# Performance work log

Hardware: AMD Instinct MI355X
Metric: run time of the kernel (lower is better)

The kernel has to match this reference:

```python
import jax, jax.numpy as jnp
import numpy as np

N = 50000      # nodes
E = 800000     # edges
IN_C = 128
HID = 96
OUT_C = 40
L = 8          # num_layers
ALPHA = 0.1
THETA = 0.5
DROPOUT = 0.5


def setup_inputs() -> dict:
    key = jax.random.key(0)
    ks = jax.random.split(key, 6)
    x = jax.random.normal(ks[0], (N, IN_C), dtype=jnp.float32)
    edge_index = jax.random.randint(ks[1], (2, E), 0, N, dtype=jnp.int64)
    proj_w = jax.random.normal(ks[2], (IN_C, HID), dtype=jnp.float32) / np.sqrt(IN_C)
    proj_b = jnp.zeros((HID,), dtype=jnp.float32)
    conv_ws = jax.random.normal(ks[3], (L, HID, HID), dtype=jnp.float32) / np.sqrt(HID)
    out_w = jax.random.normal(ks[4], (2 * HID, OUT_C), dtype=jnp.float32) / np.sqrt(2 * HID)
    out_b = jnp.zeros((OUT_C,), dtype=jnp.float32)
    return {"x": x, "edge_index": edge_index, "proj_w": proj_w, "proj_b": proj_b,
            "conv_ws": conv_ws, "out_w": out_w, "out_b": out_b}


def reference(x, edge_index, proj_w, proj_b, conv_ws, out_w, out_b):
    # --- GCN normalization with self loops (computed once, as GCN2Conv caches it) ---
    loops = jnp.arange(N, dtype=edge_index.dtype)
    src = jnp.concatenate([edge_index[0], loops])   # [E+N]
    dst = jnp.concatenate([edge_index[1], loops])
    deg = jax.ops.segment_sum(jnp.ones(E + N, dtype=x.dtype), dst, num_segments=N)
    dis = jax.lax.rsqrt(deg)                        # deg >= 1 due to self loops
    norm = dis[src] * dis[dst]                      # [E+N]

    h0 = x @ proj_w + proj_b                        # [N, HID]
    h = h0
    key = jax.random.key(42)
    for k in range(L):
        delta = 1.0 / 2 ** k
        kq, ke, kd, key = jax.random.split(key, 4)
        # dithered quantization
        b = (jax.random.uniform(kq, h.shape, dtype=h.dtype) - 0.5) * delta
        h_q = jnp.floor((h + b) / delta) * delta - b
        # GCN2Conv: propagate + initial residual + identity mapping (shared weights)
        agg = jax.ops.segment_sum(h_q[src] * norm[:, None], dst, num_segments=N)
        t = (1.0 - ALPHA) * agg + ALPHA * h0
        beta = float(np.log(THETA / (k + 1) + 1.0))
        h = (1.0 - beta) * t + beta * (t @ conv_ws[k])
        # gaussian noise + relu
        h = jax.nn.relu(h + 0.01 * jax.random.normal(ke, h.shape, dtype=h.dtype))
        if k != L - 1:
            keep = 1.0 - DROPOUT
            mask = jax.random.bernoulli(kd, keep, h.shape)
            h = jnp.where(mask, h / keep, 0.0)
    return jnp.concatenate([h0, h], axis=-1) @ out_w + out_b
```

## Files before the change

### kernel.cpp

```cpp
#include <hip/hip_runtime.h>
#include <hip/hip_fp16.h>
#include <cstdint>
#include <cmath>

#define HID 96
#define INC 128
#define OUTC 40

__device__ __forceinline__ unsigned rotl32d(unsigned x, int r){ return (x<<r)|(x>>(32-r)); }

__device__ __forceinline__ void tf2x32_dev(unsigned k0, unsigned k1, unsigned x0, unsigned x1,
                                           unsigned &y0, unsigned &y1){
  unsigned ks2 = k0 ^ k1 ^ 0x1BD11BDAu;
  x0 += k0; x1 += k1;
#define TFR(r) { x0 += x1; x1 = rotl32d(x1, r); x1 ^= x0; }
  TFR(13) TFR(15) TFR(26) TFR(6)   x0 += k1;  x1 += ks2 + 1u;
  TFR(17) TFR(29) TFR(16) TFR(24)  x0 += ks2; x1 += k0 + 2u;
  TFR(13) TFR(15) TFR(26) TFR(6)   x0 += k0;  x1 += k1 + 3u;
  TFR(17) TFR(29) TFR(16) TFR(24)  x0 += k1;  x1 += ks2 + 4u;
  TFR(13) TFR(15) TFR(26) TFR(6)   x0 += ks2; x1 += k0 + 5u;
#undef TFR
  y0 = x0; y1 = x1;
}

__device__ __forceinline__ unsigned tf_bits(unsigned k0, unsigned k1, unsigned idx){
  unsigned y0, y1; tf2x32_dev(k0, k1, 0u, idx, y0, y1); return y0 ^ y1;
}

__device__ __forceinline__ float u01_from_bits(unsigned bits){
  return __uint_as_float((bits >> 9) | 0x3f800000u) - 1.0f;
}

__device__ __forceinline__ float erfinv_xla(float x){
  float w = -log1pf(-x*x);
  float p;
  if (w < 5.0f){
    w = w - 2.5f;
    p = 2.81022636e-08f;
    p = fmaf(p,w, 3.43273939e-07f);
    p = fmaf(p,w,-3.5233877e-06f);
    p = fmaf(p,w,-4.39150654e-06f);
    p = fmaf(p,w, 0.00021858087f);
    p = fmaf(p,w,-0.00125372503f);
    p = fmaf(p,w,-0.00417768164f);
    p = fmaf(p,w, 0.246640727f);
    p = fmaf(p,w, 1.50140941f);
  } else {
    w = sqrtf(w) - 3.0f;
    p = -0.000200214257f;
    p = fmaf(p,w, 0.000100950558f);
    p = fmaf(p,w, 0.00134934322f);
    p = fmaf(p,w,-0.00367342844f);
    p = fmaf(p,w, 0.00573950773f);
    p = fmaf(p,w,-0.0076224613f);
    p = fmaf(p,w, 0.00943887047f);
    p = fmaf(p,w, 1.00167406f);
    p = fmaf(p,w, 2.83297682f);
  }
  return p*x;
}

__global__ void k_detect(const unsigned* __restrict__ raw, int* flag){
  unsigned v = raw[2*threadIdx.x + 1];
  unsigned long long m = __ballot(v == 0u);
  if (threadIdx.x == 0) *flag = (m == 0xFFFFFFFFFFFFFFFFull) ? 1 : 0;
}

__global__ void k_convcount(const unsigned* __restrict__ raw, const int* __restrict__ flag,
                            int E, int* __restrict__ src, int* __restrict__ dst,
                            int* __restrict__ cnt){
  int e = blockIdx.x*256 + threadIdx.x; if (e >= E) return;
  int s, d;
  if (*flag){ s = (int)raw[2*(size_t)e]; d = (int)raw[2*((size_t)E + e)]; }
  else      { const int* r = (const int*)raw; s = r[e]; d = r[E + e]; }
  src[e] = s; dst[e] = d;
  atomicAdd(&cnt[d], 1);
}

__global__ void k_psum_histo(const int* __restrict__ cnt, int N,
                             int* __restrict__ psum, int* __restrict__ bcnt){
  __shared__ int sh[256];
  __shared__ int lh[64];
  int tid = threadIdx.x; int n = blockIdx.x*256 + tid;
  int v = (n < N) ? cnt[n] : 0;
  sh[tid] = v;
  if (tid < 64) lh[tid] = 0;
  __syncthreads();
  if (n < N) atomicAdd(&lh[min(v, 63)], 1);
  for (int off = 128; off > 0; off >>= 1){
    __syncthreads();
    if (tid < off) sh[tid] += sh[tid + off];
  }
  __syncthreads();
  if (tid == 0) psum[blockIdx.x] = sh[0];
  if (tid < 64){
    int c = lh[tid];
    if (c > 0) atomicAdd(&bcnt[tid], c);
  }
}

__global__ void k_scan2(int* __restrict__ psum, int nb, int* __restrict__ bcnt){
  __shared__ int sh[256];
  __shared__ int sb[64];
  int tid = threadIdx.x;
  int v = (tid < nb) ? psum[tid] : 0;
  sh[tid] = v;
  if (tid < 64) sb[tid] = bcnt[tid];
  __syncthreads();
  for (int off = 1; off < 256; off <<= 1){
    int t = (tid >= off) ? sh[tid - off] : 0;
    __syncthreads();
    sh[tid] += t;
    __syncthreads();
  }
  if (tid < nb) psum[tid] = sh[tid] - v;
  if (tid < 64){
    int off = 0;
    for (int b2 = tid+1; b2 < 64; b2++) off += sb[b2];
    bcnt[tid] = off;
  }
}

__global__ void k_rowptr_perm(const int* __restrict__ cnt, const int* __restrict__ psum,
                              int N, int E, int* __restrict__ rowptr, float* __restrict__ dis,
                              int* __restrict__ bcnt, int* __restrict__ perm){
  __shared__ int sh[256];
  __shared__ int lh[64];
  int tid = threadIdx.x; int n = blockIdx.x*256 + tid;
  int v = (n < N) ? cnt[n] : 0;
  sh[tid] = v;
  if (tid < 64) lh[tid] = 0;
  __syncthreads();
  int b = min(v, 63), r = 0;
  if (n < N) r = atomicAdd(&lh[b], 1);
  for (int off = 1; off < 256; off <<= 1){
    int t = (tid >= off) ? sh[tid - off] : 0;
    __syncthreads();
    sh[tid] += t;
    __syncthreads();
  }
  if (n < N){
    rowptr[n] = psum[blockIdx.x] + sh[tid] - v;
    dis[n] = 1.0f / sqrtf((float)(v + 1));
  }
  if (n == N-1) rowptr[N] = E;
  if (tid < 64){
    int c = lh[tid];
    lh[tid] = (c > 0) ? atomicAdd(&bcnt[tid], c) : 0;
  }
  __syncthreads();
  if (n < N) perm[lh[b] + r] = n;
}

__global__ void k_fill(const int* __restrict__ src, const int* __restrict__ dst, int E,
                       const int* __restrict__ rowptr, int* __restrict__ cnt,
                       const float* __restrict__ dis,
                       int* __restrict__ csr_src, float* __restrict__ csr_w){
  int e = blockIdx.x*256 + threadIdx.x; if (e >= E) return;
  int d = dst[e], s = src[e];
  int pos = atomicAdd(&cnt[d], 1);
  int slot = rowptr[d] + pos;
  csr_src[slot] = s;
  csr_w[slot] = dis[s]*dis[d];
}

__global__ __launch_bounds__(256) void k_h0(
  const float* __restrict__ x, const float* __restrict__ W, const float* __restrict__ bias,
  float* __restrict__ h0, __half* __restrict__ hq, unsigned kq0, unsigned kq1, int N)
{
  __shared__ float xs[64*65];
  __shared__ float wsh[64*96];
  int tid = threadIdx.x; int n0 = blockIdx.x*64;
  int cg = tid & 15, ng = tid >> 4; int c0 = cg*6;
  float acc[4][6];
#pragma unroll
  for (int i=0;i<4;i++) for (int j=0;j<6;j++) acc[i][j]=0.f;
  for (int kc=0; kc<2; kc++){
    if (kc) __syncthreads();
    for (int q=tid; q<1536; q+=256)
      ((float4*)wsh)[q] = ((const float4*)(W + kc*64*96))[q];
    for (int q=tid; q<1024; q+=256){
      int g=q*4; int r=g>>6, col=g&63;
      int n=n0+r; int ns = n<N ? n : N-1;
      float4 v = ((const float4*)(x + (size_t)ns*128 + kc*64))[col>>2];
      xs[r*65+col]=v.x; xs[r*65+col+1]=v.y; xs[r*65+col+2]=v.z; xs[r*65+col+3]=v.w;
    }
    __syncthreads();
    for (int k=0;k<64;k++){
      float wv[6];
#pragma unroll
      for (int j=0;j<6;j++) wv[j]=wsh[k*96 + c0 + j];
#pragma unroll
      for (int i=0;i<4;i++){
        float xv = xs[(ng*4+i)*65 + k];
#pragma unroll
        for (int j=0;j<6;j++) acc[i][j] = fmaf(xv, wv[j], acc[i][j]);
      }
    }
  }
#pragma unroll
  for (int i=0;i<4;i++){
    int n = n0 + ng*4 + i; if (n >= N) continue;
#pragma unroll
    for (int j=0;j<6;j++){
      int c = c0 + j; int p = n*96 + c;
      float v = acc[i][j] + bias[c];
      h0[p] = v;
      unsigned bq = tf_bits(kq0, kq1, (unsigned)p);
      float b = u01_from_bits(bq) - 0.5f;
      hq[(size_t)n*96 + c] = __float2half_rn(floorf(v + b) - b);
    }
  }
}

__global__ __launch_bounds__(256, 4) void k_layer(
  const __half* __restrict__ hq_in, const float* __restrict__ h0, const float* __restrict__ dis,
  const int* __restrict__ rowptr, const int* __restrict__ csr_src, const float* __restrict__ csr_w,
  const int* __restrict__ perm, const float* __restrict__ W,
  float betaf, float ombf,
  unsigned ke0, unsigned ke1, unsigned kd0, unsigned kd1,
  unsigned kq0, unsigned kq1, float delta_n, float invdelta_n,
  int do_dropout, int write_h,
  __half* __restrict__ hq_out, float* __restrict__ h_out, int N)
{
  __shared__ float ts[64*100];
  __shared__ float wsh[24*96];
  __shared__ int rowmap[64];
  int tid = threadIdx.x;
  int tx = tid & 31, ty = tid >> 5;
  int n0 = blockIdx.x*64;

  const uint2* hq2 = (const uint2*)hq_in;
  const float4* h04 = (const float4*)h0;

#pragma unroll 1
  for (int pass = 0; pass < 8; pass++){
    int r = pass*8 + ty;
    int row = n0 + r;
    int n = (row < N) ? perm[row] : -1;
    if (tx == 0) rowmap[r] = n;
    if (tx < 24){
      float4 o = make_float4(0.f, 0.f, 0.f, 0.f);
      if (n >= 0){
        float d = dis[n];
        int lo = rowptr[n], hi = rowptr[n+1];
        uint2 sraw = hq2[(size_t)n*24 + tx];
        float2 s01 = __half22float2(*(__half2*)&sraw.x);
        float2 s23 = __half22float2(*(__half2*)&sraw.y);
        float dd = d*d;
        float ax = s01.x*dd, ay = s01.y*dd, az = s23.x*dd, aw = s23.y*dd;
        for (int s = lo; s < hi; s += 8){
          int   sn[8];
          float w[8];
#pragma unroll
          for (int j = 0; j < 8; j++){
            bool hv = (s + j) < hi;
            sn[j] = hv ? csr_src[s + j] : csr_src[s];
            w[j]  = hv ? csr_w[s + j]   : 0.0f;
          }
          uint2 g[8];
#pragma unroll
          for (int j = 0; j < 8; j++) g[j] = hq2[(size_t)sn[j]*24 + tx];
#pragma unroll
          for (int j = 0; j < 8; j++){
            float2 f01 = __half22float2(*(__half2*)&g[j].x);
            float2 f23 = __half22float2(*(__half2*)&g[j].y);
            ax = fmaf(f01.x, w[j], ax); ay = fmaf(f01.y, w[j], ay);
            az = fmaf(f23.x, w[j], az); aw = fmaf(f23.y, w[j], aw);
          }
        }
        float4 hz = h04[(size_t)n*24 + tx];
        o.x = 0.9f*ax + 0.1f*hz.x;
        o.y = 0.9f*ay + 0.1f*hz.y;
        o.z = 0.9f*az + 0.1f*hz.z;
        o.w = 0.9f*aw + 0.1f*hz.w;
      }
      *((float4*)&ts[r*100 + tx*4]) = o;
    }
  }

  int cg = tid & 7, ng = tid >> 3;
  int c0 = cg * 12;
  int r0 = ng * 2;
  float acc[2][12];
#pragma unroll
  for (int i = 0; i < 2; i++)
#pragma unroll
    for (int j = 0; j < 12; j++) acc[i][j] = 0.f;

  for (int chunk = 0; chunk < 4; chunk++){
    __syncthreads();
    for (int q = tid; q < 576; q += 256)
      ((float4*)wsh)[q] = ((const float4*)(W + chunk*24*96))[q];
    __syncthreads();
#pragma unroll 4
    for (int kk = 0; kk < 24; kk++){
      int k = chunk*24 + kk;
      float4 w0 = *((const float4*)&wsh[kk*96 + c0]);
      float4 w1 = *((const float4*)&wsh[kk*96 + c0 + 4]);
      float4 w2 = *((const float4*)&wsh[kk*96 + c0 + 8]);
      float xv0 = ts[r0*100 + k];
      float xv1 = ts[(r0+1)*100 + k];
      acc[0][0] = fmaf(xv0, w0.x, acc[0][0]);  acc[0][1] = fmaf(xv0, w0.y, acc[0][1]);
      acc[0][2] = fmaf(xv0, w0.z, acc[0][2]);  acc[0][3] = fmaf(xv0, w0.w, acc[0][3]);
      acc[0][4] = fmaf(xv0, w1.x, acc[0][4]);  acc[0][5] = fmaf(xv0, w1.y, acc[0][5]);
      acc[0][6] = fmaf(xv0, w1.z, acc[0][6]);  acc[0][7] = fmaf(xv0, w1.w, acc[0][7]);
      acc[0][8] = fmaf(xv0, w2.x, acc[0][8]);  acc[0][9] = fmaf(xv0, w2.y, acc[0][9]);
      acc[0][10]= fmaf(xv0, w2.z, acc[0][10]); acc[0][11]= fmaf(xv0, w2.w, acc[0][11]);
      acc[1][0] = fmaf(xv1, w0.x, acc[1][0]);  acc[1][1] = fmaf(xv1, w0.y, acc[1][1]);
      acc[1][2] = fmaf(xv1, w0.z, acc[1][2]);  acc[1][3] = fmaf(xv1, w0.w, acc[1][3]);
      acc[1][4] = fmaf(xv1, w1.x, acc[1][4]);  acc[1][5] = fmaf(xv1, w1.y, acc[1][5]);
      acc[1][6] = fmaf(xv1, w1.z, acc[1][6]);  acc[1][7] = fmaf(xv1, w1.w, acc[1][7]);
      acc[1][8] = fmaf(xv1, w2.x, acc[1][8]);  acc[1][9] = fmaf(xv1, w2.y, acc[1][9]);
      acc[1][10]= fmaf(xv1, w2.z, acc[1][10]); acc[1][11]= fmaf(xv1, w2.w, acc[1][11]);
    }
  }

  const float LO = __uint_as_float(0xBF7FFFFFu);
#pragma unroll
  for (int i = 0; i < 2; i++){
    int n = rowmap[r0 + i]; if (n < 0) continue;
    float res[12];
#pragma unroll
    for (int j = 0; j < 12; j++){
      int c = c0 + j; int p = n*96 + c;
      float tv = ts[(r0+i)*100 + c];
      float hv = ombf*tv + betaf*acc[i][j];
      unsigned be = tf_bits(ke0, ke1, (unsigned)p);
      float uv = fmaxf(LO, u01_from_bits(be)*2.0f + LO);
      hv += 0.01f * (1.41421356f * erfinv_xla(uv));
      hv = fmaxf(hv, 0.0f);
      if (do_dropout){
        unsigned bd = tf_bits(kd0, kd1, (unsigned)p);
        hv = (bd < 0x80000000u) ? hv*2.0f : 0.0f;
      }
      if (!write_h){
        unsigned bq = tf_bits(kq0, kq1, (unsigned)p);
        float b = (u01_from_bits(bq) - 0.5f)*delta_n;
        hv = floorf((hv + b)*invdelta_n)*delta_n - b;
      }
      res[j] = hv;
    }
    if (write_h){
      float* dst = h_out + (size_t)n*96 + c0;
#pragma unroll
      for (int j4 = 0; j4 < 3; j4++)
        *((float4*)&dst[j4*4]) = make_float4(res[j4*4], res[j4*4+1], res[j4*4+2], res[j4*4+3]);
    } else {
      uint2* dst = (uint2*)(hq_out + (size_t)n*96 + c0);
#pragma unroll
      for (int j4 = 0; j4 < 3; j4++){
        unsigned lo2 = (unsigned)__half_as_ushort(__float2half_rn(res[j4*4+0]))
                     | ((unsigned)__half_as_ushort(__float2half_rn(res[j4*4+1])) << 16);
        unsigned hi2 = (unsigned)__half_as_ushort(__float2half_rn(res[j4*4+2]))
                     | ((unsigned)__half_as_ushort(__float2half_rn(res[j4*4+3])) << 16);
        dst[j4] = make_uint2(lo2, hi2);
      }
    }
  }
}

__global__ __launch_bounds__(256) void k_final(
  const float* __restrict__ h0, const float* __restrict__ h,
  const float* __restrict__ W, const float* __restrict__ bias,
  float* __restrict__ out, int N)
{
  __shared__ float xs[64*97];
  __shared__ float wsh[96*40];
  int tid = threadIdx.x; int n0 = blockIdx.x*64;
  int cg = tid & 7, ng = tid >> 3; int c0 = cg*5;
  float acc[2][5];
#pragma unroll
  for (int i=0;i<2;i++) for (int j=0;j<5;j++) acc[i][j]=0.f;
  for (int ph=0; ph<2; ph++){
    if (ph) __syncthreads();
    const float* xsrc = ph ? h : h0;
    for (int q=tid; q<960; q+=256)
      ((float4*)wsh)[q] = ((const float4*)(W + ph*96*40))[q];
    for (int q=tid; q<1536; q+=256){
      int g=q*4; int r=g/96, col=g%96;
      int n=n0+r; int ns = n<N ? n : N-1;
      float4 v = ((const float4*)(xsrc + (size_t)ns*96))[col>>2];
      xs[r*97+col]=v.x; xs[r*97+col+1]=v.y; xs[r*97+col+2]=v.z; xs[r*97+col+3]=v.w;
    }
    __syncthreads();
    for (int k=0;k<96;k++){
      float wv[5];
#pragma unroll
      for (int j=0;j<5;j++) wv[j]=wsh[k*40 + c0 + j];
#pragma unroll
      for (int i=0;i<2;i++){
        float xv = xs[(ng*2+i)*97 + k];
#pragma unroll
        for (int j=0;j<5;j++) acc[i][j] = fmaf(xv, wv[j], acc[i][j]);
      }
    }
  }
#pragma unroll
  for (int i=0;i<2;i++){
    int n = n0 + ng*2 + i; if (n >= N) continue;
#pragma unroll
    for (int j=0;j<5;j++)
      out[(size_t)n*40 + c0 + j] = acc[i][j] + bias[c0 + j];
  }
}

static void tf_host(uint32_t k0, uint32_t k1, uint32_t x0, uint32_t x1,
                    uint32_t &y0, uint32_t &y1){
  uint32_t ks2 = k0 ^ k1 ^ 0x1BD11BDAu;
  x0 += k0; x1 += k1;
  auto R = [&](int r){ x0 += x1; x1 = (x1<<r)|(x1>>(32-r)); x1 ^= x0; };
  R(13);R(15);R(26);R(6);   x0 += k1;  x1 += ks2 + 1u;
  R(17);R(29);R(16);R(24);  x0 += ks2; x1 += k0 + 2u;
  R(13);R(15);R(26);R(6);   x0 += k0;  x1 += k1 + 3u;
  R(17);R(29);R(16);R(24);  x0 += k1;  x1 += ks2 + 4u;
  R(13);R(15);R(26);R(6);   x0 += ks2; x1 += k0 + 5u;
  y0 = x0; y1 = x1;
}

extern "C" void kernel_launch(void* const* d_in, const int* in_sizes, int n_in,
                              void* d_out, int out_size, void* d_ws, size_t ws_size,
                              hipStream_t stream)
{
  const float*    x       = (const float*)d_in[0];
  const unsigned* eraw    = (const unsigned*)d_in[1];
  const float*    proj_w  = (const float*)d_in[2];
  const float*    proj_b  = (const float*)d_in[3];
  const float*    conv_w  = (const float*)d_in[4];
  const float*    out_w   = (const float*)d_in[5];
  const float*    out_b   = (const float*)d_in[6];
  float* out = (float*)d_out;

  const int N = in_sizes[0] / INC;
  const int E = in_sizes[1] / 2;
  const size_t NH = (size_t)N * HID;

  float*  ws     = (float*)d_ws;
  float*  h0     = ws;
  __half* hqA    = (__half*)(h0 + NH);
  __half* hqB    = hqA + NH;
  float*  hb     = (float*)(hqB + NH);
  float*  dis    = hb + NH;
  int*    cnt    = (int*)(dis + N);
  int*    rowptr = cnt + N;
  int*    csr_src= rowptr + (N + 1);
  float*  csr_w  = (float*)(csr_src + E);
  int*    srcb   = (int*)(csr_w + E);
  int*    dstb   = srcb + E;
  int*    flag   = dstb + E;
  int*    perm   = flag + 1;
  int*    bcnt   = perm + N;
  int*    psum   = bcnt + 64;
  (void)ws_size; (void)n_in; (void)out_size;

  uint32_t kq[8][2], ke[8][2], kd[8][2];
  {
    uint32_t K0 = 0u, K1 = 42u;
    for (int k = 0; k < 8; k++){
      uint32_t y0, y1;
      tf_host(K0, K1, 0u, 0u, y0, y1); kq[k][0]=y0; kq[k][1]=y1;
      tf_host(K0, K1, 0u, 1u, y0, y1); ke[k][0]=y0; ke[k][1]=y1;
      tf_host(K0, K1, 0u, 2u, y0, y1); kd[k][0]=y0; kd[k][1]=y1;
      tf_host(K0, K1, 0u, 3u, y0, y1); K0=y0; K1=y1;
    }
  }

  const int gE  = (E + 255)/256;
  const int gN  = (N + 255)/256;
  const int gMM = (N + 63)/64;

  hipMemsetAsync(cnt, 0, (size_t)N*4, stream);
  hipMemsetAsync(bcnt, 0, 64*4, stream);
  k_detect <<<1, 64, 0, stream>>>(eraw, flag);
  k_convcount<<<gE, 256, 0, stream>>>(eraw, flag, E, srcb, dstb, cnt);
  k_psum_histo<<<gN, 256, 0, stream>>>(cnt, N, psum, bcnt);
  k_scan2  <<<1, 256, 0, stream>>>(psum, gN, bcnt);
  k_rowptr_perm<<<gN, 256, 0, stream>>>(cnt, psum, N, E, rowptr, dis, bcnt, perm);
  hipMemsetAsync(cnt, 0, (size_t)N*4, stream);
  k_fill   <<<gE, 256, 0, stream>>>(srcb, dstb, E, rowptr, cnt, dis, csr_src, csr_w);

  k_h0<<<gMM, 256, 0, stream>>>(x, proj_w, proj_b, h0, hqA, kq[0][0], kq[0][1], N);

  for (int k = 0; k < 8; k++){
    double bd = log(0.5/(double)(k+1) + 1.0);
    float betaf = (float)bd;
    float ombf  = (float)(1.0 - bd);
    int last = (k == 7);
    float dn  = 1.0f/(float)(1 << (k+1));
    float idn = (float)(1 << (k+1));
    const __half* hin  = (k & 1) ? hqB : hqA;
    __half*       hout = (k & 1) ? hqA : hqB;
    k_layer<<<gMM, 256, 0, stream>>>(hin, h0, dis, rowptr, csr_src, csr_w, perm,
      conv_w + (size_t)k*HID*HID, betaf, ombf,
      ke[k][0], ke[k][1], kd[k][0], kd[k][1],
      last?0u:kq[k+1][0], last?0u:kq[k+1][1], dn, idn,
      !last, last, hout, hb, N);
  }

  k_final<<<gMM, 256, 0, stream>>>(h0, hb, out_w, out_b, out, N);
}
```

Before: 0.9996 ms.

## Pad CSR rows to multiples of eight and shrink layer tiles to 32 rows

CSR rows are padded to a multiple of 8 with zero-weight dummy entries, so the gather loop can use aligned int4/float4 loads without bounds checks and 32-bit offset arithmetic. The src/dst staging buffers are removed, and k_fill reads raw edge indices directly. k_layer now processes 32 rows per block with one row per thread group in the matmul, and launch bounds are raised for more occupancy. Padding adds up to 7 extra dummy gathers per node.

New measurement: 977.1 us. 2.3% less time.

```diff
diff --git a/kernel.cpp b/kernel.cpp
--- a/kernel.cpp
+++ b/kernel.cpp
@@ -6,6 +6,7 @@
 #define HID 96
 #define INC 128
 #define OUTC 40
+#define ROWS 32
 
 __device__ __forceinline__ unsigned rotl32d(unsigned x, int r){ return (x<<r)|(x>>(32-r)); }
 
@@ -67,13 +68,11 @@
 }
 
 __global__ void k_convcount(const unsigned* __restrict__ raw, const int* __restrict__ flag,
-                            int E, int* __restrict__ src, int* __restrict__ dst,
-                            int* __restrict__ cnt){
+                            int E, int* __restrict__ cnt){
   int e = blockIdx.x*256 + threadIdx.x; if (e >= E) return;
-  int s, d;
-  if (*flag){ s = (int)raw[2*(size_t)e]; d = (int)raw[2*((size_t)E + e)]; }
-  else      { const int* r = (const int*)raw; s = r[e]; d = r[E + e]; }
-  src[e] = s; dst[e] = d;
+  int d;
+  if (*flag) d = (int)raw[2*((size_t)E + e)];
+  else       d = ((const int*)raw)[E + e];
   atomicAdd(&cnt[d], 1);
 }
 
@@ -83,7 +82,8 @@
   __shared__ int lh[64];
   int tid = threadIdx.x; int n = blockIdx.x*256 + tid;
   int v = (n < N) ? cnt[n] : 0;
-  sh[tid] = v;
+  int vp = (v + 7) & ~7;
+  sh[tid] = vp;
   if (tid < 64) lh[tid] = 0;
   __syncthreads();
   if (n < N) atomicAdd(&lh[min(v, 63)], 1);
@@ -122,13 +122,15 @@
 }
 
 __global__ void k_rowptr_perm(const int* __restrict__ cnt, const int* __restrict__ psum,
-                              int N, int E, int* __restrict__ rowptr, float* __restrict__ dis,
-                              int* __restrict__ bcnt, int* __restrict__ perm){
+                              int N, int* __restrict__ rowptr, float* __restrict__ dis,
+                              int* __restrict__ bcnt, int* __restrict__ perm,
+                              int* __restrict__ csr_src, float* __restrict__ csr_w){
   __shared__ int sh[256];
   __shared__ int lh[64];
   int tid = threadIdx.x; int n = blockIdx.x*256 + tid;
   int v = (n < N) ? cnt[n] : 0;
-  sh[tid] = v;
+  int vp = (v + 7) & ~7;
+  sh[tid] = vp;
   if (tid < 64) lh[tid] = 0;
   __syncthreads();
   int b = min(v, 63), r = 0;
@@ -140,10 +142,12 @@
     __syncthreads();
   }
   if (n < N){
-    rowptr[n] = psum[blockIdx.x] + sh[tid] - v;
+    int rp = psum[blockIdx.x] + sh[tid] - vp;
+    rowptr[n] = rp;
     dis[n] = 1.0f / sqrtf((float)(v + 1));
-  }
-  if (n == N-1) rowptr[N] = E;
+    for (int q = v; q < vp; q++){ csr_src[rp + q] = 0; csr_w[rp + q] = 0.0f; }
+    if (n == N-1) rowptr[N] = rp + vp;
+  }
   if (tid < 64){
     int c = lh[tid];
     lh[tid] = (c > 0) ? atomicAdd(&bcnt[tid], c) : 0;
@@ -152,12 +156,14 @@
   if (n < N) perm[lh[b] + r] = n;
 }
 
-__global__ void k_fill(const int* __restrict__ src, const int* __restrict__ dst, int E,
+__global__ void k_fill(const unsigned* __restrict__ raw, const int* __restrict__ flag, int E,
                        const int* __restrict__ rowptr, int* __restrict__ cnt,
                        const float* __restrict__ dis,
                        int* __restrict__ csr_src, float* __restrict__ csr_w){
   int e = blockIdx.x*256 + threadIdx.x; if (e >= E) return;
-  int d = dst[e], s = src[e];
+  int s, d;
+  if (*flag){ s = (int)raw[2*(size_t)e]; d = (int)raw[2*((size_t)E + e)]; }
+  else      { const int* r = (const int*)raw; s = r[e]; d = r[E + e]; }
   int pos = atomicAdd(&cnt[d], 1);
   int slot = rowptr[d] + pos;
   csr_src[slot] = s;
@@ -213,7 +219,13 @@
   }
 }
 
-__global__ __launch_bounds__(256, 4) void k_layer(
+#define GATH(gj, wv) { \
+  float2 f01 = __half22float2(*(__half2*)&gj.x); \
+  float2 f23 = __half22float2(*(__half2*)&gj.y); \
+  ax = fmaf(f01.x, wv, ax); ay = fmaf(f01.y, wv, ay); \
+  az = fmaf(f23.x, wv, az); aw = fmaf(f23.y, wv, aw); }
+
+__global__ __launch_bounds__(256, 6) void k_layer(
   const __half* __restrict__ hq_in, const float* __restrict__ h0, const float* __restrict__ dis,
   const int* __restrict__ rowptr, const int* __restrict__ csr_src, const float* __restrict__ csr_w,
   const int* __restrict__ perm, const float* __restrict__ W,
@@ -223,18 +235,18 @@
   int do_dropout, int write_h,
   __half* __restrict__ hq_out, float* __restrict__ h_out, int N)
 {
-  __shared__ float ts[64*100];
+  __shared__ float ts[ROWS*100];
   __shared__ float wsh[24*96];
-  __shared__ int rowmap[64];
+  __shared__ int rowmap[ROWS];
   int tid = threadIdx.x;
   int tx = tid & 31, ty = tid >> 5;
-  int n0 = blockIdx.x*64;
-
-  const uint2* hq2 = (const uint2*)hq_in;
-  const float4* h04 = (const float4*)h0;
+  int n0 = blockIdx.x*ROWS;
+
+  const char* hqc = (const char*)hq_in;
+  const char* h0c = (const char*)h0;
 
 #pragma unroll 1
-  for (int pass = 0; pass < 8; pass++){
+  for (int pass = 0; pass < 4; pass++){
     int r = pass*8 + ty;
     int row = n0 + r;
     int n = (row < N) ? perm[row] : -1;
@@ -243,33 +255,30 @@
       float4 o = make_float4(0.f, 0.f, 0.f, 0.f);
       if (n >= 0){
         float d = dis[n];
-        int lo = rowptr[n], hi = rowptr[n+1];
-        uint2 sraw = hq2[(size_t)n*24 + tx];
+        unsigned lo = (unsigned)rowptr[n], hi = (unsigned)rowptr[n+1];
+        unsigned txb = (unsigned)tx*8u;
+        uint2 sraw = *(const uint2*)(hqc + (unsigned)n*192u + txb);
         float2 s01 = __half22float2(*(__half2*)&sraw.x);
         float2 s23 = __half22float2(*(__half2*)&sraw.y);
         float dd = d*d;
         float ax = s01.x*dd, ay = s01.y*dd, az = s23.x*dd, aw = s23.y*dd;
-        for (int s = lo; s < hi; s += 8){
-          int   sn[8];
-          float w[8];
-#pragma unroll
-          for (int j = 0; j < 8; j++){
-            bool hv = (s + j) < hi;
-            sn[j] = hv ? csr_src[s + j] : csr_src[s];
-            w[j]  = hv ? csr_w[s + j]   : 0.0f;
-          }
-          uint2 g[8];
-#pragma unroll
-          for (int j = 0; j < 8; j++) g[j] = hq2[(size_t)sn[j]*24 + tx];
-#pragma unroll
-          for (int j = 0; j < 8; j++){
-            float2 f01 = __half22float2(*(__half2*)&g[j].x);
-            float2 f23 = __half22float2(*(__half2*)&g[j].y);
-            ax = fmaf(f01.x, w[j], ax); ay = fmaf(f01.y, w[j], ay);
-            az = fmaf(f23.x, w[j], az); aw = fmaf(f23.y, w[j], aw);
-          }
+        for (unsigned s = lo; s < hi; s += 8){
+          int4   sa = *(const int4*)(csr_src + s);
+          int4   sb = *(const int4*)(csr_src + s + 4);
+          float4 wa = *(const float4*)(csr_w + s);
+          float4 wb = *(const float4*)(csr_w + s + 4);
+          uint2 g0 = *(const uint2*)(hqc + (unsigned)sa.x*192u + txb);
+          uint2 g1 = *(const uint2*)(hqc + (unsigned)sa.y*192u + txb);
+          uint2 g2 = *(const uint2*)(hqc + (unsigned)sa.z*192u + txb);
+          uint2 g3 = *(const uint2*)(hqc + (unsigned)sa.w*192u + txb);
+          uint2 g4 = *(const uint2*)(hqc + (unsigned)sb.x*192u + txb);
+          uint2 g5 = *(const uint2*)(hqc + (unsigned)sb.y*192u + txb);
+          uint2 g6 = *(const uint2*)(hqc + (unsigned)sb.z*192u + txb);
+          uint2 g7 = *(const uint2*)(hqc + (unsigned)sb.w*192u + txb);
+          GATH(g0, wa.x) GATH(g1, wa.y) GATH(g2, wa.z) GATH(g3, wa.w)
+          GATH(g4, wb.x) GATH(g5, wb.y) GATH(g6, wb.z) GATH(g7, wb.w)
         }
-        float4 hz = h04[(size_t)n*24 + tx];
+        float4 hz = *(const float4*)(h0c + (unsigned)n*384u + (unsigned)tx*16u);
         o.x = 0.9f*ax + 0.1f*hz.x;
         o.y = 0.9f*ay + 0.1f*hz.y;
         o.z = 0.9f*az + 0.1f*hz.z;
@@ -281,12 +290,9 @@
 
   int cg = tid & 7, ng = tid >> 3;
   int c0 = cg * 12;
-  int r0 = ng * 2;
-  float acc[2][12];
-#pragma unroll
-  for (int i = 0; i < 2; i++)
-#pragma unroll
-    for (int j = 0; j < 12; j++) acc[i][j] = 0.f;
+  float acc[12];
+#pragma unroll
+  for (int j = 0; j < 12; j++) acc[j] = 0.f;
 
   for (int chunk = 0; chunk < 4; chunk++){
     __syncthreads();
@@ -299,62 +305,54 @@
       float4 w0 = *((const float4*)&wsh[kk*96 + c0]);
       float4 w1 = *((const float4*)&wsh[kk*96 + c0 + 4]);
       float4 w2 = *((const float4*)&wsh[kk*96 + c0 + 8]);
-      float xv0 = ts[r0*100 + k];
-      float xv1 = ts[(r0+1)*100 + k];
-      acc[0][0] = fmaf(xv0, w0.x, acc[0][0]);  acc[0][1] = fmaf(xv0, w0.y, acc[0][1]);
-      acc[0][2] = fmaf(xv0, w0.z, acc[0][2]);  acc[0][3] = fmaf(xv0, w0.w, acc[0][3]);
-      acc[0][4] = fmaf(xv0, w1.x, acc[0][4]);  acc[0][5] = fmaf(xv0, w1.y, acc[0][5]);
-      acc[0][6] = fmaf(xv0, w1.z, acc[0][6]);  acc[0][7] = fmaf(xv0, w1.w, acc[0][7]);
-      acc[0][8] = fmaf(xv0, w2.x, acc[0][8]);  acc[0][9] = fmaf(xv0, w2.y, acc[0][9]);
-      acc[0][10]= fmaf(xv0, w2.z, acc[0][10]); acc[0][11]= fmaf(xv0, w2.w, acc[0][11]);
-      acc[1][0] = fmaf(xv1, w0.x, acc[1][0]);  acc[1][1] = fmaf(xv1, w0.y, acc[1][1]);
-      acc[1][2] = fmaf(xv1, w0.z, acc[1][2]);  acc[1][3] = fmaf(xv1, w0.w, acc[1][3]);
-      acc[1][4] = fmaf(xv1, w1.x, acc[1][4]);  acc[1][5] = fmaf(xv1, w1.y, acc[1][5]);
-      acc[1][6] = fmaf(xv1, w1.z, acc[1][6]);  acc[1][7] = fmaf(xv1, w1.w, acc[1][7]);
-      acc[1][8] = fmaf(xv1, w2.x, acc[1][8]);  acc[1][9] = fmaf(xv1, w2.y, acc[1][9]);
-      acc[1][10]= fmaf(xv1, w2.z, acc[1][10]); acc[1][11]= fmaf(xv1, w2.w, acc[1][11]);
+      float xv = ts[ng*100 + k];
+      acc[0] = fmaf(xv, w0.x, acc[0]);  acc[1] = fmaf(xv, w0.y, acc[1]);
+      acc[2] = fmaf(xv, w0.z, acc[2]);  acc[3] = fmaf(xv, w0.w, acc[3]);
+      acc[4] = fmaf(xv, w1.x, acc[4]);  acc[5] = fmaf(xv, w1.y, acc[5]);
+      acc[6] = fmaf(xv, w1.z, acc[6]);  acc[7] = fmaf(xv, w1.w, acc[7]);
+      acc[8] = fmaf(xv, w2.x, acc[8]);  acc[9] = fmaf(xv, w2.y, acc[9]);
+      acc[10]= fmaf(xv, w2.z, acc[10]); acc[11]= fmaf(xv, w2.w, acc[11]);
     }
   }
 
   const float LO = __uint_as_float(0xBF7FFFFFu);
-#pragma unroll
-  for (int i = 0; i < 2; i++){
-    int n = rowmap[r0 + i]; if (n < 0) continue;
+  int n = rowmap[ng];
+  if (n >= 0){
     float res[12];
 #pragma unroll
     for (int j = 0; j < 12; j++){
-      int c = c0 + j; int p = n*96 + c;
-      float tv = ts[(r0+i)*100 + c];
-      float hv = ombf*tv + betaf*acc[i][j];
-      unsigned be = tf_bits(ke0, ke1, (unsigned)p);
+      int c = c0 + j; unsigned p = (unsigned)n*96u + (unsigned)c;
+      float tv = ts[ng*100 + c];
+      float hv = ombf*tv + betaf*acc[j];
+      unsigned be = tf_bits(ke0, ke1, p);
       float uv = fmaxf(LO, u01_from_bits(be)*2.0f + LO);
       hv += 0.01f * (1.41421356f * erfinv_xla(uv));
       hv = fmaxf(hv, 0.0f);
       if (do_dropout){
-        unsigned bd = tf_bits(kd0, kd1, (unsigned)p);
+        unsigned bd = tf_bits(kd0, kd1, p);
         hv = (bd < 0x80000000u) ? hv*2.0f : 0.0f;
       }
       if (!write_h){
-        unsigned bq = tf_bits(kq0, kq1, (unsigned)p);
+        unsigned bq = tf_bits(kq0, kq1, p);
         float b = (u01_from_bits(bq) - 0.5f)*delta_n;
         hv = floorf((hv + b)*invdelta_n)*delta_n - b;
       }
       res[j] = hv;
     }
     if (write_h){
-      float* dst = h_out + (size_t)n*96 + c0;
+      float* dst2 = h_out + (size_t)n*96 + c0;
 #pragma unroll
       for (int j4 = 0; j4 < 3; j4++)
-        *((float4*)&dst[j4*4]) = make_float4(res[j4*4], res[j4*4+1], res[j4*4+2], res[j4*4+3]);
+        *((float4*)&dst2[j4*4]) = make_float4(res[j4*4], res[j4*4+1], res[j4*4+2], res[j4*4+3]);
     } else {
-      uint2* dst = (uint2*)(hq_out + (size_t)n*96 + c0);
+      uint2* dst2 = (uint2*)(hq_out + (size_t)n*96 + c0);
 #pragma unroll
       for (int j4 = 0; j4 < 3; j4++){
         unsigned lo2 = (unsigned)__half_as_ushort(__float2half_rn(res[j4*4+0]))
                      | ((unsigned)__half_as_ushort(__float2half_rn(res[j4*4+1])) << 16);
         unsigned hi2 = (unsigned)__half_as_ushort(__float2half_rn(res[j4*4+2]))
                      | ((unsigned)__half_as_ushort(__float2half_rn(res[j4*4+3])) << 16);
-        dst[j4] = make_uint2(lo2, hi2);
+        dst2[j4] = make_uint2(lo2, hi2);
       }
     }
   }
@@ -434,6 +432,7 @@
   const int N = in_sizes[0] / INC;
   const int E = in_sizes[1] / 2;
   const size_t NH = (size_t)N * HID;
+  const int EP = ((E + 7*N + 15) & ~15);
 
   float*  ws     = (float*)d_ws;
   float*  h0     = ws;
@@ -443,13 +442,11 @@
   float*  dis    = hb + NH;
   int*    cnt    = (int*)(dis + N);
   int*    rowptr = cnt + N;
-  int*    csr_src= rowptr + (N + 1);
-  float*  csr_w  = (float*)(csr_src + E);
-  int*    srcb   = (int*)(csr_w + E);
-  int*    dstb   = srcb + E;
-  int*    flag   = dstb + E;
-  int*    perm   = flag + 1;
-  int*    bcnt   = perm + N;
+  int*    csr_src= rowptr + ((N + 16) & ~15);
+  float*  csr_w  = (float*)(csr_src + EP);
+  int*    flag   = (int*)(csr_w + EP);
+  int*    perm   = flag + 16;
+  int*    bcnt   = perm + ((N + 15) & ~15);
   int*    psum   = bcnt + 64;
   (void)ws_size; (void)n_in; (void)out_size;
 
@@ -468,16 +465,17 @@
   const int gE  = (E + 255)/256;
   const int gN  = (N + 255)/256;
   const int gMM = (N + 63)/64;
+  const int gL  = (N + ROWS-1)/ROWS;
 
   hipMemsetAsync(cnt, 0, (size_t)N*4, stream);
   hipMemsetAsync(bcnt, 0, 64*4, stream);
   k_detect <<<1, 64, 0, stream>>>(eraw, flag);
-  k_convcount<<<gE, 256, 0, stream>>>(eraw, flag, E, srcb, dstb, cnt);
+  k_convcount<<<gE, 256, 0, stream>>>(eraw, flag, E, cnt);
   k_psum_histo<<<gN, 256, 0, stream>>>(cnt, N, psum, bcnt);
   k_scan2  <<<1, 256, 0, stream>>>(psum, gN, bcnt);
-  k_rowptr_perm<<<gN, 256, 0, stream>>>(cnt, psum, N, E, rowptr, dis, bcnt, perm);
+  k_rowptr_perm<<<gN, 256, 0, stream>>>(cnt, psum, N, rowptr, dis, bcnt, perm, csr_src, csr_w);
   hipMemsetAsync(cnt, 0, (size_t)N*4, stream);
-  k_fill   <<<gE, 256, 0, stream>>>(srcb, dstb, E, rowptr, cnt, dis, csr_src, csr_w);
+  k_fill   <<<gE, 256, 0, stream>>>(eraw, flag, E, rowptr, cnt, dis, csr_src, csr_w);
 
   k_h0<<<gMM, 256, 0, stream>>>(x, proj_w, proj_b, h0, hqA, kq[0][0], kq[0][1], N);
 
@@ -490,7 +488,7 @@
     float idn = (float)(1 << (k+1));
     const __half* hin  = (k & 1) ? hqB : hqA;
     __half*       hout = (k & 1) ? hqA : hqB;
-    k_layer<<<gMM, 256, 0, stream>>>(hin, h0, dis, rowptr, csr_src, csr_w, perm,
+    k_layer<<<gL, 256, 0, stream>>>(hin, h0, dis, rowptr, csr_src, csr_w, perm,
       conv_w + (size_t)k*HID*HID, betaf, ombf,
       ke[k][0], ke[k][1], kd[k][0], kd[k][1],
       last?0u:kq[k+1][0], last?0u:kq[k+1][1], dn, idn,
```
